# Optimization experiments

Hardware: AMD Instinct MI355X
Metric: run time of the kernel (lower is better)

## Reference

```python
import jax, jax.numpy as jnp
import numpy as np

B, L, DN, DE, DD, H = 2, 512, 512, 128, 128, 8
DK, DEH, DDH = DN // H, DE // H, DD // H
F = 2 * DK + DEH + 2 * DDH  # per-head concat feature size (176)
SLOPE = 0.2


def _kaiming(key, out_f, in_f):
    bound = np.sqrt(6.0 / ((1.0 + SLOPE ** 2) * in_f))
    return jax.random.uniform(key, (out_f, in_f), minval=-bound, maxval=bound, dtype=jnp.float32)


def lin(x, w, b):
    y = jnp.einsum('...i,oi->...o', x, w)
    return y if b is None else y + b


def setup_inputs() -> dict:
    key = jax.random.key(0)
    ks = jax.random.split(key, 16)
    inp = {
        'node_representation': jax.random.normal(ks[0], (B, L, DN), dtype=jnp.float32),
        'edge_representation': jax.random.normal(ks[1], (B, L, L, DE), dtype=jnp.float32),
        'diff_vec': jax.random.normal(ks[2], (B, L, DD), dtype=jnp.float32),
        'Wn_w': _kaiming(ks[3], DN, DN), 'Wn_b': jnp.zeros((DN,), jnp.float32),
        'We_w': _kaiming(ks[4], DE, DE), 'We_b': jnp.zeros((DE,), jnp.float32),
        'Wd_w': _kaiming(ks[5], DD, DD), 'Wd_b': jnp.zeros((DD,), jnp.float32),
        'Wh_w': _kaiming(ks[6], DK, DK), 'Wh_b': jnp.zeros((DK,), jnp.float32),
        'attn_w': _kaiming(ks[7], 1, F),
        'outn_w': _kaiming(ks[8], DN, DN), 'outn_b': jnp.zeros((DN,), jnp.float32),
        'Wn2_w': _kaiming(ks[9], DN, DN), 'Wn2_b': jnp.zeros((DN,), jnp.float32),
        'We2_w': _kaiming(ks[10], DE, DE), 'We2_b': jnp.zeros((DE,), jnp.float32),
        'Wd2_w': _kaiming(ks[11], DD, DD), 'Wd2_b': jnp.zeros((DD,), jnp.float32),
        'edge_w': _kaiming(ks[12], DEH, F), 'edge_b': jnp.zeros((DEH,), jnp.float32),
        'oute_w': _kaiming(ks[13], DE, DE), 'oute_b': jnp.zeros((DE,), jnp.float32),
    }
    return inp


def reference(node_representation, edge_representation, diff_vec,
              Wn_w, Wn_b, We_w, We_b, Wd_w, Wd_b, Wh_w, Wh_b, attn_w,
              outn_w, outn_b, Wn2_w, Wn2_b, We2_w, We2_b, Wd2_w, Wd2_b,
              edge_w, edge_b, oute_w, oute_b):
    lrelu = lambda x: jax.nn.leaky_relu(x, SLOPE)

    # ---- node update (GAT-style with concat score decomposed per term) ----
    npj = lin(node_representation, Wn_w, Wn_b).reshape(B, L, H, DK)
    epj = lin(edge_representation, We_w, We_b).reshape(B, L, L, H, DEH)
    dpj = lin(diff_vec, Wd_w, Wd_b).reshape(B, L, H, DDH)
    a = attn_w[0]  # concat order: [hi, hj, edge, di, dj]
    a_hi, a_hj = a[:DK], a[DK:2 * DK]
    a_e = a[2 * DK:2 * DK + DEH]
    a_di, a_dj = a[2 * DK + DEH:2 * DK + DEH + DDH], a[-DDH:]
    # scores[b,i,j,h]
    s = (jnp.einsum('blhd,d->blh', npj, a_hi)[:, :, None, :]
         + jnp.einsum('blhd,d->blh', npj, a_hj)[:, None, :, :]
         + jnp.einsum('blmhe,e->blmh', epj, a_e)
         + jnp.einsum('blhd,d->blh', dpj, a_di)[:, :, None, :]
         + jnp.einsum('blhd,d->blh', dpj, a_dj)[:, None, :, :])
    diag = jnp.eye(L, dtype=bool)[None, :, :, None]
    s = jnp.where(diag, -jnp.inf, s)
    probs = jax.nn.softmax(lrelu(s), axis=2)  # softmax over j
    node_wh = lin(npj, Wh_w, Wh_b)  # [B,L,H,DK]
    agg = jnp.einsum('blmh,bmhd->blhd', probs, node_wh)
    new_node = (npj + lrelu(agg)).reshape(B, L, DN)
    new_node = lin(new_node, outn_w, outn_b)

    # ---- edge update (concat-linear decomposed into per-term matmuls) ----
    np2 = lin(new_node, Wn2_w, Wn2_b).reshape(B, L, H, DK)
    ep2 = lin(edge_representation, We2_w, We2_b).reshape(B, L, L, H, DEH)
    dp2 = lin(diff_vec, Wd2_w, Wd2_b).reshape(B, L, H, DDH)
    # edge concat order: [edge, hi, hj, di, dj]
    W_e = edge_w[:, :DEH]
    W_hi = edge_w[:, DEH:DEH + DK]
    W_hj = edge_w[:, DEH + DK:DEH + 2 * DK]
    W_di = edge_w[:, DEH + 2 * DK:DEH + 2 * DK + DDH]
    W_dj = edge_w[:, -DDH:]
    e_out = (jnp.einsum('blmhe,fe->blmhf', ep2, W_e)
             + jnp.einsum('blhd,fd->blhf', np2, W_hi)[:, :, None]
             + jnp.einsum('blhd,fd->blhf', np2, W_hj)[:, None]
             + jnp.einsum('blhd,fd->blhf', dp2, W_di)[:, :, None]
             + jnp.einsum('blhd,fd->blhf', dp2, W_dj)[:, None]
             + edge_b)
    new_edge = lin(e_out.reshape(B, L, L, DE), oute_w, oute_b)
    return new_node, new_edge
```

## Files before the change

kernel.cpp:

```cpp
#include <hip/hip_runtime.h>
#include <hip/hip_bf16.h>

typedef unsigned short u16;
typedef unsigned short u16x8 __attribute__((ext_vector_type(8)));
typedef __bf16 bf16x8 __attribute__((ext_vector_type(8)));
typedef float f32x4 __attribute__((ext_vector_type(4)));

#define LRS 0.2f

__device__ __forceinline__ u16 f2b(float f) {
  __hip_bfloat16 h = __float2bfloat16(f);
  return __builtin_bit_cast(u16, h);
}

template<int K, int O, int KSEG>
__device__ __forceinline__ void gemm_rows4(const float* xr, const float* W, const float* bias,
                                           float* yl, float* yg, int ygstride) {
  constexpr int KPT = K / KSEG;
  constexpr int OPP = 256 / KSEG;
  const int t = threadIdx.x;
  const int ks = t % KSEG;
  const int oi = t / KSEG;
#pragma unroll
  for (int pass = 0; pass < O / OPP; ++pass) {
    const int o = pass * OPP + oi;
    float a0 = 0, a1 = 0, a2 = 0, a3 = 0;
    const float* wp = W + (size_t)o * K + ks * KPT;
    const float* xb = xr + ks * KPT;
#pragma unroll 4
    for (int kc = 0; kc < KPT; kc += 4) {
      f32x4 w4 = *(const f32x4*)(wp + kc);
      const float* xp = xb + kc;
#pragma unroll
      for (int j = 0; j < 4; ++j) {
        float w = w4[j];
        a0 += xp[j] * w;
        a1 += xp[K + j] * w;
        a2 += xp[2 * K + j] * w;
        a3 += xp[3 * K + j] * w;
      }
    }
#pragma unroll
    for (int d = 1; d < KSEG; d <<= 1) {
      a0 += __shfl_xor(a0, d, 64);
      a1 += __shfl_xor(a1, d, 64);
      a2 += __shfl_xor(a2, d, 64);
      a3 += __shfl_xor(a3, d, 64);
    }
    if (ks == 0) {
      float bv = bias ? bias[o] : 0.0f;
      float v0 = a0 + bv, v1 = a1 + bv, v2 = a2 + bv, v3 = a3 + bv;
      if (yl) { yl[o] = v0; yl[O + o] = v1; yl[2 * O + o] = v2; yl[3 * O + o] = v3; }
      if (yg) { yg[o] = v0; yg[ygstride + o] = v1; yg[2 * (size_t)ygstride + o] = v2; yg[3 * (size_t)ygstride + o] = v3; }
    }
  }
}

__global__ __launch_bounds__(256) void kW1(const float* We_w, const float* We_b, const float* attn,
                                           const float* We2_w, const float* We2_b,
                                           const float* edge_w, const float* edge_b,
                                           float* Mfull, u16* vb, float* cbe, float* sconst) {
  int gid = blockIdx.x * 256 + threadIdx.x;
  if (gid < 16384) {
    int hf = gid >> 7, c = gid & 127;
    int h = hf >> 4, fo = hf & 15;
    float s = 0;
    for (int e = 0; e < 16; ++e)
      s += edge_w[fo * 176 + e] * We2_w[(h * 16 + e) * 128 + c];
    Mfull[hf * 128 + c] = s;
  } else if (gid < 16384 + 2048) {
    int idx = gid - 16384;
    int c = idx >> 4, hc = idx & 15;
    float s = 0;
    if (hc < 8)
      for (int e = 0; e < 16; ++e)
        s += We_w[(hc * 16 + e) * 128 + c] * attn[128 + e];
    vb[c * 16 + hc] = f2b(s);
  } else if (gid < 18432 + 128) {
    int hf = gid - 18432;
    int h = hf >> 4, fo = hf & 15;
    float s = edge_b[fo];
    for (int e = 0; e < 16; ++e)
      s += We2_b[h * 16 + e] * edge_w[fo * 176 + e];
    cbe[hf] = s;
  } else if (gid < 18560 + 8) {
    int h = gid - 18560;
    float s = 0;
    for (int e = 0; e < 16; ++e)
      s += We_b[h * 16 + e] * attn[128 + e];
    sconst[h] = s;
  }
}

__global__ __launch_bounds__(256) void kW2(const float* oute_w, const float* Mfull, u16* Gb) {
  int gid = blockIdx.x * 256 + threadIdx.x;
  int o = gid >> 7, c = gid & 127;
  float s = 0;
  for (int k = 0; k < 128; ++k)
    s += oute_w[o * 128 + k] * Mfull[k * 128 + c];
  Gb[o * 128 + c] = f2b(s);
}

__global__ __launch_bounds__(256) void kN1(const float* node, const float* diff,
                                           const float* Wn_w, const float* Wn_b,
                                           const float* Wd_w, const float* Wd_b,
                                           const float* Wh_w, const float* Wh_b,
                                           const float* attn, const float* sconst,
                                           float* npj_g, float* nwh_g,
                                           float* srow_g, float* scol_g) {
  __shared__ float nrow[4 * 512], npjl[4 * 512], drow[4 * 128], dpjl[4 * 128];
  const int t = threadIdx.x;
  const int r0 = blockIdx.x * 4;
  *(f32x4*)&nrow[t * 8]     = *(const f32x4*)(node + (size_t)r0 * 512 + t * 8);
  *(f32x4*)&nrow[t * 8 + 4] = *(const f32x4*)(node + (size_t)r0 * 512 + t * 8 + 4);
  if (t < 64) {
    *(f32x4*)&drow[t * 8]     = *(const f32x4*)(diff + (size_t)r0 * 128 + t * 8);
    *(f32x4*)&drow[t * 8 + 4] = *(const f32x4*)(diff + (size_t)r0 * 128 + t * 8 + 4);
  }
  __syncthreads();
  gemm_rows4<512, 512, 4>(nrow, Wn_w, Wn_b, npjl, npj_g + (size_t)r0 * 512, 512);
  gemm_rows4<128, 128, 4>(drow, Wd_w, Wd_b, dpjl, nullptr, 0);
  __syncthreads();
  {
    int d = t & 63, hh = t >> 6;
#pragma unroll
    for (int hi = 0; hi < 2; ++hi) {
      int h = hh + hi * 4;
      float wb = Wh_b[d];
      float acc[4] = {wb, wb, wb, wb};
      for (int k = 0; k < 64; ++k) {
        float w = Wh_w[d * 64 + k];
#pragma unroll
        for (int r = 0; r < 4; ++r) acc[r] += npjl[r * 512 + h * 64 + k] * w;
      }
#pragma unroll
      for (int r = 0; r < 4; ++r) nwh_g[(size_t)(r0 + r) * 512 + h * 64 + d] = acc[r];
    }
  }
  if (t < 32) {
    int r = t >> 3, h = t & 7;
    float shi = 0, shj = 0, sdi = 0, sdj = 0;
    for (int d = 0; d < 64; ++d) {
      float x = npjl[r * 512 + h * 64 + d];
      shi += x * attn[d];
      shj += x * attn[64 + d];
    }
    for (int e = 0; e < 16; ++e) {
      float x = dpjl[r * 128 + h * 16 + e];
      sdi += x * attn[144 + e];
      sdj += x * attn[160 + e];
    }
    srow_g[(r0 + r) * 8 + h] = shi + sdi + sconst[h];
    scol_g[(r0 + r) * 8 + h] = shj + sdj;
  }
}

__global__ __launch_bounds__(256) void kA(const float* edge, const float* npj, const float* nwh,
                                          const float* srow, const float* scol,
                                          const u16* vb, float* nnp) {
  __shared__ float s_arr[512][9];
  __shared__ float red[256];
  __shared__ float mxh[8], inv8[8];
  __shared__ float part[2][512];
  const int bl = blockIdx.x;
  const int b = bl >> 9, l = bl & 511;
  const int t = threadIdx.x;
  const int w = t >> 6, lane = t & 63;
  const int colL = lane & 15, kg = lane >> 4;
  bf16x8 bfr[4];
#pragma unroll
  for (int ks = 0; ks < 4; ++ks) {
    u16x8 u;
#pragma unroll
    for (int j = 0; j < 8; ++j) u[j] = vb[(ks * 32 + kg * 8 + j) * 16 + colL];
    bfr[ks] = __builtin_bit_cast(bf16x8, u);
  }
  float srh = (colL < 8) ? srow[(size_t)bl * 8 + colL] : 0.0f;
  const float* erow = edge + (size_t)bl * 512 * 128;
  for (int fr = 0; fr < 8; ++fr) {
    int m0 = w * 128 + fr * 16;
    f32x4 acc = {0, 0, 0, 0};
#pragma unroll
    for (int ks = 0; ks < 4; ++ks) {
      const float* ep = erow + (size_t)(m0 + colL) * 128 + ks * 32 + kg * 8;
      f32x4 e0 = *(const f32x4*)(ep);
      f32x4 e1 = *(const f32x4*)(ep + 4);
      u16x8 a8;
#pragma unroll
      for (int j = 0; j < 4; ++j) { a8[j] = f2b(e0[j]); a8[4 + j] = f2b(e1[j]); }
      acc = __builtin_amdgcn_mfma_f32_16x16x32_bf16(__builtin_bit_cast(bf16x8, a8), bfr[ks], acc, 0, 0, 0);
    }
    if (colL < 8) {
#pragma unroll
      for (int r = 0; r < 4; ++r) {
        int m = m0 + kg * 4 + r;
        float sv = acc[r] + srh + scol[((size_t)b * 512 + m) * 8 + colL];
        sv = (m == l) ? -__builtin_inff() : (sv >= 0.0f ? sv : LRS * sv);
        s_arr[m][colL] = sv;
      }
    }
  }
  __syncthreads();
  const int h = t & 7, seg = t >> 3;
  float mx = -__builtin_inff();
#pragma unroll 4
  for (int i = 0; i < 16; ++i) mx = fmaxf(mx, s_arr[seg * 16 + i][h]);
  red[t] = mx;
  __syncthreads();
  if (t < 8) {
    float m2 = -__builtin_inff();
    for (int sg = 0; sg < 32; ++sg) m2 = fmaxf(m2, red[sg * 8 + t]);
    mxh[t] = m2;
  }
  __syncthreads();
  float mh = mxh[h];
  float sm = 0;
#pragma unroll 4
  for (int i = 0; i < 16; ++i) {
    int m = seg * 16 + i;
    float p = __expf(s_arr[m][h] - mh);
    s_arr[m][h] = p;
    sm += p;
  }
  red[t] = sm;
  __syncthreads();
  if (t < 8) {
    float s2 = 0;
    for (int sg = 0; sg < 32; ++sg) s2 += red[sg * 8 + t];
    inv8[t] = 1.0f / s2;
  }
  __syncthreads();
  const int half = t >> 7, oq = t & 127;
  const int o4 = oq * 4, hh = oq >> 4;
  f32x4 acc4 = {0, 0, 0, 0};
  const float* nb = nwh + (size_t)b * 512 * 512;
  for (int m = half * 256; m < half * 256 + 256; ++m) {
    float p = s_arr[m][hh];
    f32x4 nv = *(const f32x4*)(nb + (size_t)m * 512 + o4);
    acc4 += p * nv;
  }
  *(f32x4*)&part[half][o4] = acc4;
  __syncthreads();
  if (t < 128) {
    int ob = t * 4, h2 = t >> 4;
    f32x4 s0 = *(f32x4*)&part[0][ob];
    f32x4 s1 = *(f32x4*)&part[1][ob];
    f32x4 np4 = *(const f32x4*)(npj + (size_t)bl * 512 + ob);
    float iv = inv8[h2];
    f32x4 o;
#pragma unroll
    for (int j = 0; j < 4; ++j) {
      float a = (s0[j] + s1[j]) * iv;
      a = a >= 0.0f ? a : LRS * a;
      o[j] = np4[j] + a;
    }
    *(f32x4*)(nnp + (size_t)bl * 512 + ob) = o;
  }
}

__global__ __launch_bounds__(256) void kN2(const float* nnp, const float* outn_w, const float* outn_b,
                                           float* out0) {
  __shared__ float xr[4 * 512];
  const int t = threadIdx.x;
  const int r0 = blockIdx.x * 4;
  *(f32x4*)&xr[t * 4]        = *(const f32x4*)(nnp + (size_t)r0 * 512 + t * 4);
  *(f32x4*)&xr[1024 + t * 4] = *(const f32x4*)(nnp + (size_t)r0 * 512 + 1024 + t * 4);
  __syncthreads();
  gemm_rows4<512, 512, 4>(xr, outn_w, outn_b, nullptr, out0 + (size_t)r0 * 512, 512);
}

__global__ __launch_bounds__(256) void kN3(const float* nn, const float* diff,
                                           const float* Wn2_w, const float* Wn2_b,
                                           const float* Wd2_w, const float* Wd2_b,
                                           const float* edge_w, const float* cbe,
                                           float* Rl_g, float* Rm_g) {
  __shared__ float xr[4 * 512], np2l[4 * 512], dr[4 * 128], dp2l[4 * 128];
  const int t = threadIdx.x;
  const int r0 = blockIdx.x * 4;
  *(f32x4*)&xr[t * 4]        = *(const f32x4*)(nn + (size_t)r0 * 512 + t * 4);
  *(f32x4*)&xr[1024 + t * 4] = *(const f32x4*)(nn + (size_t)r0 * 512 + 1024 + t * 4);
  if (t < 64) {
    *(f32x4*)&dr[t * 8]     = *(const f32x4*)(diff + (size_t)r0 * 128 + t * 8);
    *(f32x4*)&dr[t * 8 + 4] = *(const f32x4*)(diff + (size_t)r0 * 128 + t * 8 + 4);
  }
  __syncthreads();
  gemm_rows4<512, 512, 4>(xr, Wn2_w, Wn2_b, np2l, nullptr, 0);
  gemm_rows4<128, 128, 4>(dr, Wd2_w, Wd2_b, dp2l, nullptr, 0);
  __syncthreads();
  {
    int hf = t & 127, which = t >> 7;
    int h = hf >> 4, fo = hf & 15;
    const float* wh = edge_w + fo * 176 + 16 + which * 64;
    const float* wd = edge_w + fo * 176 + 144 + which * 16;
    float add = which ? 0.0f : cbe[hf];
    float* dst = which ? Rm_g : Rl_g;
#pragma unroll
    for (int r = 0; r < 4; ++r) {
      float a = add;
      for (int d = 0; d < 64; ++d) a += np2l[r * 512 + h * 64 + d] * wh[d];
      for (int e = 0; e < 16; ++e) a += dp2l[r * 128 + h * 16 + e] * wd[e];
      dst[(size_t)(r0 + r) * 128 + hf] = a;
    }
  }
}

__global__ __launch_bounds__(256) void kN4(const float* Rl, const float* Rm,
                                           const float* oute_w, const float* oute_b,
                                           float* Pl, float* Pm) {
  __shared__ float xl[4 * 128], xm[4 * 128];
  const int t = threadIdx.x;
  const int r0 = blockIdx.x * 4;
  if (t < 128) *(f32x4*)&xl[t * 4] = *(const f32x4*)(Rl + (size_t)r0 * 128 + t * 4);
  else { int q = t - 128; *(f32x4*)&xm[q * 4] = *(const f32x4*)(Rm + (size_t)r0 * 128 + q * 4); }
  __syncthreads();
  gemm_rows4<128, 128, 4>(xl, oute_w, oute_b, nullptr, Pl + (size_t)r0 * 128, 128);
  gemm_rows4<128, 128, 4>(xm, oute_w, nullptr, nullptr, Pm + (size_t)r0 * 128, 128);
}

__global__ __launch_bounds__(256) void kE(const float* edge, const u16* Gb,
                                          const float* Pl, const float* Pm, float* oute) {
  __shared__ u16 At[16384];
  __shared__ u16 Gt[16384];
  const int tile = blockIdx.x;
  const int bl = tile >> 2;
  const int b = bl >> 9;
  const int m0 = (tile & 3) * 128;
  const int t = threadIdx.x, lane = t & 63, w = t >> 6;
  const float* Ab = edge + ((size_t)bl * 512 + m0) * 128;
#pragma unroll
  for (int j = 0; j < 8; ++j) {
    int u = j * 256 + t;
    int row = u >> 4, cu = u & 15;
    int su = row * 16 + (cu ^ (row & 7));
    f32x4 e0 = *(const f32x4*)(Ab + (size_t)row * 128 + cu * 8);
    f32x4 e1 = *(const f32x4*)(Ab + (size_t)row * 128 + cu * 8 + 4);
    u16x8 a8;
#pragma unroll
    for (int j2 = 0; j2 < 4; ++j2) { a8[j2] = f2b(e0[j2]); a8[4 + j2] = f2b(e1[j2]); }
    *(u16x8*)(At + su * 8) = a8;
    *(u16x8*)(Gt + su * 8) = *(const u16x8*)(Gb + u * 8);
  }
  __syncthreads();
  const int wr = w >> 1, wc = w & 1;
  const int colL = lane & 15, kg = lane >> 4;
  f32x4 acc[4][4] = {};
#pragma unroll
  for (int ks = 0; ks < 4; ++ks) {
    bf16x8 af[4], bfv[4];
    int cu = ks * 4 + kg;
#pragma unroll
    for (int i = 0; i < 4; ++i) {
      int row = wr * 64 + i * 16 + colL;
      af[i] = *(bf16x8*)(At + (row * 16 + (cu ^ (row & 7))) * 8);
      int orow = wc * 64 + i * 16 + colL;
      bfv[i] = *(bf16x8*)(Gt + (orow * 16 + (cu ^ (orow & 7))) * 8);
    }
#pragma unroll
    for (int i = 0; i < 4; ++i)
#pragma unroll
      for (int n = 0; n < 4; ++n)
        acc[i][n] = __builtin_amdgcn_mfma_f32_16x16x32_bf16(af[i], bfv[n], acc[i][n], 0, 0, 0);
  }
  const float* plp = Pl + (size_t)bl * 128;
  float plv[4];
#pragma unroll
  for (int n = 0; n < 4; ++n) plv[n] = plp[wc * 64 + n * 16 + colL];
  float* ob = oute + ((size_t)bl * 512 + m0) * 128;
#pragma unroll
  for (int i = 0; i < 4; ++i) {
#pragma unroll
    for (int r = 0; r < 4; ++r) {
      int m = wr * 64 + i * 16 + kg * 4 + r;
      const float* pmp = Pm + ((size_t)b * 512 + m0 + m) * 128;
#pragma unroll
      for (int n = 0; n < 4; ++n) {
        int o = wc * 64 + n * 16 + colL;
        ob[(size_t)m * 128 + o] = acc[i][n][r] + plv[n] + pmp[o];
      }
    }
  }
}

extern "C" void kernel_launch(void* const* d_in, const int* in_sizes, int n_in,
                              void* d_out, int out_size, void* d_ws, size_t ws_size,
                              hipStream_t stream) {
  (void)in_sizes; (void)n_in; (void)out_size; (void)ws_size;
  const float* node   = (const float*)d_in[0];
  const float* edge   = (const float*)d_in[1];
  const float* diff   = (const float*)d_in[2];
  const float* Wn_w   = (const float*)d_in[3];
  const float* Wn_b   = (const float*)d_in[4];
  const float* We_w   = (const float*)d_in[5];
  const float* We_b   = (const float*)d_in[6];
  const float* Wd_w   = (const float*)d_in[7];
  const float* Wd_b   = (const float*)d_in[8];
  const float* Wh_w   = (const float*)d_in[9];
  const float* Wh_b   = (const float*)d_in[10];
  const float* attn   = (const float*)d_in[11];
  const float* outn_w = (const float*)d_in[12];
  const float* outn_b = (const float*)d_in[13];
  const float* Wn2_w  = (const float*)d_in[14];
  const float* Wn2_b  = (const float*)d_in[15];
  const float* We2_w  = (const float*)d_in[16];
  const float* We2_b  = (const float*)d_in[17];
  const float* Wd2_w  = (const float*)d_in[18];
  const float* Wd2_b  = (const float*)d_in[19];
  const float* edge_w = (const float*)d_in[20];
  const float* edge_b = (const float*)d_in[21];
  const float* oute_w = (const float*)d_in[22];
  const float* oute_b = (const float*)d_in[23];

  float* out0 = (float*)d_out;
  float* out1 = out0 + 524288;

  float* f = (float*)d_ws;
  size_t off = 0;
  auto alloc = [&](size_t n) { float* p = f + off; off += (n + 7) & ~(size_t)7; return p; };
  float* npj    = alloc(524288);
  float* nwh    = alloc(524288);
  float* srow   = alloc(8192);
  float* scol   = alloc(8192);
  float* sconst = alloc(8);
  float* cbe    = alloc(128);
  float* Mfull  = alloc(16384);
  float* nnp    = alloc(524288);
  float* Rl     = alloc(131072);
  float* Rm     = alloc(131072);
  float* Pl     = alloc(131072);
  float* Pm     = alloc(131072);
  u16* vb = (u16*)(f + off); off += 1024;
  u16* Gb = (u16*)(f + off); off += 8192;

  hipLaunchKernelGGL(kW1, dim3(73), dim3(256), 0, stream,
                     We_w, We_b, attn, We2_w, We2_b, edge_w, edge_b, Mfull, vb, cbe, sconst);
  hipLaunchKernelGGL(kW2, dim3(64), dim3(256), 0, stream, oute_w, Mfull, Gb);
  hipLaunchKernelGGL(kN1, dim3(256), dim3(256), 0, stream,
                     node, diff, Wn_w, Wn_b, Wd_w, Wd_b, Wh_w, Wh_b, attn, sconst,
                     npj, nwh, srow, scol);
  hipLaunchKernelGGL(kA, dim3(1024), dim3(256), 0, stream,
                     edge, npj, nwh, srow, scol, vb, nnp);
  hipLaunchKernelGGL(kN2, dim3(256), dim3(256), 0, stream, nnp, outn_w, outn_b, out0);
  hipLaunchKernelGGL(kN3, dim3(256), dim3(256), 0, stream,
                     out0, diff, Wn2_w, Wn2_b, Wd2_w, Wd2_b, edge_w, cbe, Rl, Rm);
  hipLaunchKernelGGL(kN4, dim3(256), dim3(256), 0, stream, Rl, Rm, oute_w, oute_b, Pl, Pm);
  hipLaunchKernelGGL(kE, dim3(4096), dim3(256), 0, stream, edge, Gb, Pl, Pm, out1);
}
```

Measured before the change: 445.8 us.

## Use fp32 FMA edge scores in kA and double-buffer edge tiles in kE

kA drops the bf16 MFMA edge-score path and computes the per-head edge scores with fp32 FMAs and shuffle reductions, prefetching the next edge row while computing. The leaky-relu and masking step moves into the max pass, and the weighted sum over nodes is split across two accumulators. kE now runs one block per row l, looping over 8 tiles of 64 rows with a double-buffered LDS A-tile and register prefetch, so Gt is loaded once per block instead of four times and loads overlap with MFMA. Risks are lower occupancy and more VALU work in kA, and fewer blocks in kE.

After: 494.0 us. 1.11x slower.

```diff
diff --git a/kernel.cpp b/kernel.cpp
--- a/kernel.cpp
+++ b/kernel.cpp
@@ -59,7 +59,7 @@
 __global__ __launch_bounds__(256) void kW1(const float* We_w, const float* We_b, const float* attn,
                                            const float* We2_w, const float* We2_b,
                                            const float* edge_w, const float* edge_b,
-                                           float* Mfull, u16* vb, float* cbe, float* sconst) {
+                                           float* Mfull, float* vf, float* cbe, float* sconst) {
   int gid = blockIdx.x * 256 + threadIdx.x;
   if (gid < 16384) {
     int hf = gid >> 7, c = gid & 127;
@@ -71,11 +71,12 @@
   } else if (gid < 16384 + 2048) {
     int idx = gid - 16384;
     int c = idx >> 4, hc = idx & 15;
-    float s = 0;
-    if (hc < 8)
+    if (hc < 8) {
+      float s = 0;
       for (int e = 0; e < 16; ++e)
         s += We_w[(hc * 16 + e) * 128 + c] * attn[128 + e];
-    vb[c * 16 + hc] = f2b(s);
+      vf[c * 8 + hc] = s;
+    }
   } else if (gid < 18432 + 128) {
     int hf = gid - 18432;
     int h = hf >> 4, fo = hf & 15;
@@ -157,7 +158,7 @@
 
 __global__ __launch_bounds__(256) void kA(const float* edge, const float* npj, const float* nwh,
                                           const float* srow, const float* scol,
-                                          const u16* vb, float* nnp) {
+                                          const float* vf, float* nnp) {
   __shared__ float s_arr[512][9];
   __shared__ float red[256];
   __shared__ float mxh[8], inv8[8];
@@ -165,46 +166,60 @@
   const int bl = blockIdx.x;
   const int b = bl >> 9, l = bl & 511;
   const int t = threadIdx.x;
-  const int w = t >> 6, lane = t & 63;
-  const int colL = lane & 15, kg = lane >> 4;
-  bf16x8 bfr[4];
-#pragma unroll
-  for (int ks = 0; ks < 4; ++ks) {
-    u16x8 u;
-#pragma unroll
-    for (int j = 0; j < 8; ++j) u[j] = vb[(ks * 32 + kg * 8 + j) * 16 + colL];
-    bfr[ks] = __builtin_bit_cast(bf16x8, u);
-  }
-  float srh = (colL < 8) ? srow[(size_t)bl * 8 + colL] : 0.0f;
-  const float* erow = edge + (size_t)bl * 512 * 128;
-  for (int fr = 0; fr < 8; ++fr) {
-    int m0 = w * 128 + fr * 16;
-    f32x4 acc = {0, 0, 0, 0};
-#pragma unroll
-    for (int ks = 0; ks < 4; ++ks) {
-      const float* ep = erow + (size_t)(m0 + colL) * 128 + ks * 32 + kg * 8;
-      f32x4 e0 = *(const f32x4*)(ep);
-      f32x4 e1 = *(const f32x4*)(ep + 4);
-      u16x8 a8;
-#pragma unroll
-      for (int j = 0; j < 4; ++j) { a8[j] = f2b(e0[j]); a8[4 + j] = f2b(e1[j]); }
-      acc = __builtin_amdgcn_mfma_f32_16x16x32_bf16(__builtin_bit_cast(bf16x8, a8), bfr[ks], acc, 0, 0, 0);
-    }
-    if (colL < 8) {
-#pragma unroll
-      for (int r = 0; r < 4; ++r) {
-        int m = m0 + kg * 4 + r;
-        float sv = acc[r] + srh + scol[((size_t)b * 512 + m) * 8 + colL];
-        sv = (m == l) ? -__builtin_inff() : (sv >= 0.0f ? sv : LRS * sv);
-        s_arr[m][colL] = sv;
-      }
-    }
-  }
-  __syncthreads();
+
+  {
+    const int sub = t & 15, rg = t >> 4;
+    f32x4 vrx[16];
+#pragma unroll
+    for (int q = 0; q < 16; ++q) vrx[q] = *(const f32x4*)(vf + sub * 64 + q * 4);
+    const float* ebase = edge + (size_t)bl * 65536 + (size_t)rg * 128 + sub * 8;
+    f32x4 c0 = *(const f32x4*)ebase;
+    f32x4 c1 = *(const f32x4*)(ebase + 4);
+    for (int it = 0; it < 32; ++it) {
+      f32x4 n0, n1;
+      if (it < 31) {
+        const float* ep = ebase + (size_t)(it + 1) * 2048;
+        n0 = *(const f32x4*)ep;
+        n1 = *(const f32x4*)(ep + 4);
+      }
+      float acc[8];
+#pragma unroll
+      for (int h2 = 0; h2 < 8; ++h2) acc[h2] = 0.0f;
+#pragma unroll
+      for (int j = 0; j < 4; ++j) {
+#pragma unroll
+        for (int h2 = 0; h2 < 8; ++h2) {
+          acc[h2] += c0[j] * vrx[j * 2 + (h2 >> 2)][h2 & 3];
+          acc[h2] += c1[j] * vrx[8 + j * 2 + (h2 >> 2)][h2 & 3];
+        }
+      }
+#pragma unroll
+      for (int d = 1; d < 16; d <<= 1) {
+#pragma unroll
+        for (int h2 = 0; h2 < 8; ++h2) acc[h2] += __shfl_xor(acc[h2], d, 64);
+      }
+      if (sub < 8) {
+        float a = acc[0];
+#pragma unroll
+        for (int h2 = 1; h2 < 8; ++h2) if (sub == h2) a = acc[h2];
+        s_arr[it * 16 + rg][sub] = a;
+      }
+      if (it < 31) { c0 = n0; c1 = n1; }
+    }
+  }
+  __syncthreads();
+
   const int h = t & 7, seg = t >> 3;
+  const float srh2 = srow[(size_t)bl * 8 + h];
   float mx = -__builtin_inff();
 #pragma unroll 4
-  for (int i = 0; i < 16; ++i) mx = fmaxf(mx, s_arr[seg * 16 + i][h]);
+  for (int i = 0; i < 16; ++i) {
+    int m = seg * 16 + i;
+    float sv = s_arr[m][h] + srh2 + scol[((size_t)b * 512 + m) * 8 + h];
+    sv = (m == l) ? -__builtin_inff() : (sv >= 0.0f ? sv : LRS * sv);
+    s_arr[m][h] = sv;
+    mx = fmaxf(mx, sv);
+  }
   red[t] = mx;
   __syncthreads();
   if (t < 8) {
@@ -230,16 +245,16 @@
     inv8[t] = 1.0f / s2;
   }
   __syncthreads();
+
   const int half = t >> 7, oq = t & 127;
   const int o4 = oq * 4, hh = oq >> 4;
-  f32x4 acc4 = {0, 0, 0, 0};
+  f32x4 acc4a = {0, 0, 0, 0}, acc4b = {0, 0, 0, 0};
   const float* nb = nwh + (size_t)b * 512 * 512;
-  for (int m = half * 256; m < half * 256 + 256; ++m) {
-    float p = s_arr[m][hh];
-    f32x4 nv = *(const f32x4*)(nb + (size_t)m * 512 + o4);
-    acc4 += p * nv;
-  }
-  *(f32x4*)&part[half][o4] = acc4;
+  for (int m = half * 256; m < half * 256 + 256; m += 2) {
+    acc4a += s_arr[m][hh]     * *(const f32x4*)(nb + (size_t)m * 512 + o4);
+    acc4b += s_arr[m + 1][hh] * *(const f32x4*)(nb + (size_t)(m + 1) * 512 + o4);
+  }
+  *(f32x4*)&part[half][o4] = acc4a + acc4b;
   __syncthreads();
   if (t < 128) {
     int ob = t * 4, h2 = t >> 4;
@@ -319,65 +334,92 @@
 
 __global__ __launch_bounds__(256) void kE(const float* edge, const u16* Gb,
                                           const float* Pl, const float* Pm, float* oute) {
-  __shared__ u16 At[16384];
   __shared__ u16 Gt[16384];
-  const int tile = blockIdx.x;
-  const int bl = tile >> 2;
+  __shared__ u16 At[2][8192];
+  const int bl = blockIdx.x;
   const int b = bl >> 9;
-  const int m0 = (tile & 3) * 128;
   const int t = threadIdx.x, lane = t & 63, w = t >> 6;
-  const float* Ab = edge + ((size_t)bl * 512 + m0) * 128;
-#pragma unroll
-  for (int j = 0; j < 8; ++j) {
-    int u = j * 256 + t;
+  const float* Ab = edge + (size_t)bl * 65536;
+  const int arow = t >> 2, aseg = t & 3;
+
+  f32x4 pf[8];
+  auto issueA = [&](int tile) {
+    const float* p = Ab + (size_t)(tile * 64 + arow) * 128 + aseg * 32;
+#pragma unroll
+    for (int q = 0; q < 8; ++q) pf[q] = *(const f32x4*)(p + q * 4);
+  };
+  auto writeA = [&](int buf) {
+#pragma unroll
+    for (int jj = 0; jj < 4; ++jj) {
+      u16x8 a8;
+#pragma unroll
+      for (int j2 = 0; j2 < 4; ++j2) {
+        a8[j2]     = f2b(pf[2 * jj][j2]);
+        a8[4 + j2] = f2b(pf[2 * jj + 1][j2]);
+      }
+      int cu = aseg * 4 + jj;
+      *(u16x8*)(At[buf] + (arow * 16 + (cu ^ (arow & 7))) * 8) = a8;
+    }
+  };
+
+  issueA(0);
+#pragma unroll
+  for (int i2 = 0; i2 < 8; ++i2) {
+    int u = i2 * 256 + t;
     int row = u >> 4, cu = u & 15;
-    int su = row * 16 + (cu ^ (row & 7));
-    f32x4 e0 = *(const f32x4*)(Ab + (size_t)row * 128 + cu * 8);
-    f32x4 e1 = *(const f32x4*)(Ab + (size_t)row * 128 + cu * 8 + 4);
-    u16x8 a8;
-#pragma unroll
-    for (int j2 = 0; j2 < 4; ++j2) { a8[j2] = f2b(e0[j2]); a8[4 + j2] = f2b(e1[j2]); }
-    *(u16x8*)(At + su * 8) = a8;
-    *(u16x8*)(Gt + su * 8) = *(const u16x8*)(Gb + u * 8);
-  }
-  __syncthreads();
+    *(u16x8*)(Gt + (row * 16 + (cu ^ (row & 7))) * 8) = *(const u16x8*)(Gb + u * 8);
+  }
+  writeA(0);
+  __syncthreads();
+
   const int wr = w >> 1, wc = w & 1;
   const int colL = lane & 15, kg = lane >> 4;
-  f32x4 acc[4][4] = {};
-#pragma unroll
-  for (int ks = 0; ks < 4; ++ks) {
-    bf16x8 af[4], bfv[4];
-    int cu = ks * 4 + kg;
-#pragma unroll
-    for (int i = 0; i < 4; ++i) {
-      int row = wr * 64 + i * 16 + colL;
-      af[i] = *(bf16x8*)(At + (row * 16 + (cu ^ (row & 7))) * 8);
-      int orow = wc * 64 + i * 16 + colL;
-      bfv[i] = *(bf16x8*)(Gt + (orow * 16 + (cu ^ (orow & 7))) * 8);
-    }
-#pragma unroll
-    for (int i = 0; i < 4; ++i)
-#pragma unroll
-      for (int n = 0; n < 4; ++n)
-        acc[i][n] = __builtin_amdgcn_mfma_f32_16x16x32_bf16(af[i], bfv[n], acc[i][n], 0, 0, 0);
-  }
   const float* plp = Pl + (size_t)bl * 128;
   float plv[4];
 #pragma unroll
   for (int n = 0; n < 4; ++n) plv[n] = plp[wc * 64 + n * 16 + colL];
-  float* ob = oute + ((size_t)bl * 512 + m0) * 128;
-#pragma unroll
-  for (int i = 0; i < 4; ++i) {
-#pragma unroll
-    for (int r = 0; r < 4; ++r) {
-      int m = wr * 64 + i * 16 + kg * 4 + r;
-      const float* pmp = Pm + ((size_t)b * 512 + m0 + m) * 128;
+
+  for (int tile = 0; tile < 8; ++tile) {
+    if (tile < 7) issueA(tile + 1);
+    const int buf = tile & 1;
+    f32x4 acc[2][4] = {};
+#pragma unroll
+    for (int ks = 0; ks < 4; ++ks) {
+      int cu = ks * 4 + kg;
+      bf16x8 af[2], bfv[4];
+#pragma unroll
+      for (int i = 0; i < 2; ++i) {
+        int row = wr * 32 + i * 16 + colL;
+        af[i] = *(bf16x8*)(At[buf] + (row * 16 + (cu ^ (row & 7))) * 8);
+      }
 #pragma unroll
       for (int n = 0; n < 4; ++n) {
-        int o = wc * 64 + n * 16 + colL;
-        ob[(size_t)m * 128 + o] = acc[i][n][r] + plv[n] + pmp[o];
-      }
-    }
+        int orow = wc * 64 + n * 16 + colL;
+        bfv[n] = *(bf16x8*)(Gt + (orow * 16 + (cu ^ (orow & 7))) * 8);
+      }
+#pragma unroll
+      for (int i = 0; i < 2; ++i)
+#pragma unroll
+        for (int n = 0; n < 4; ++n)
+          acc[i][n] = __builtin_amdgcn_mfma_f32_16x16x32_bf16(af[i], bfv[n], acc[i][n], 0, 0, 0);
+    }
+    if (tile < 7) writeA(buf ^ 1);
+    const int m0 = tile * 64;
+    float* ob = oute + ((size_t)bl * 512 + m0) * 128;
+#pragma unroll
+    for (int i = 0; i < 2; ++i) {
+#pragma unroll
+      for (int r = 0; r < 4; ++r) {
+        int m = wr * 32 + i * 16 + kg * 4 + r;
+        const float* pmp = Pm + ((size_t)b * 512 + m0 + m) * 128;
+#pragma unroll
+        for (int n = 0; n < 4; ++n) {
+          int o = wc * 64 + n * 16 + colL;
+          ob[(size_t)m * 128 + o] = acc[i][n][r] + plv[n] + pmp[o];
+        }
+      }
+    }
+    __syncthreads();
   }
 }
 
@@ -428,20 +470,20 @@
   float* Rm     = alloc(131072);
   float* Pl     = alloc(131072);
   float* Pm     = alloc(131072);
-  u16* vb = (u16*)(f + off); off += 1024;
+  float* vf     = alloc(1024);
   u16* Gb = (u16*)(f + off); off += 8192;
 
   hipLaunchKernelGGL(kW1, dim3(73), dim3(256), 0, stream,
-                     We_w, We_b, attn, We2_w, We2_b, edge_w, edge_b, Mfull, vb, cbe, sconst);
+                     We_w, We_b, attn, We2_w, We2_b, edge_w, edge_b, Mfull, vf, cbe, sconst);
   hipLaunchKernelGGL(kW2, dim3(64), dim3(256), 0, stream, oute_w, Mfull, Gb);
   hipLaunchKernelGGL(kN1, dim3(256), dim3(256), 0, stream,
                      node, diff, Wn_w, Wn_b, Wd_w, Wd_b, Wh_w, Wh_b, attn, sconst,
                      npj, nwh, srow, scol);
   hipLaunchKernelGGL(kA, dim3(1024), dim3(256), 0, stream,
-                     edge, npj, nwh, srow, scol, vb, nnp);
+                     edge, npj, nwh, srow, scol, vf, nnp);
   hipLaunchKernelGGL(kN2, dim3(256), dim3(256), 0, stream, nnp, outn_w, outn_b, out0);
   hipLaunchKernelGGL(kN3, dim3(256), dim3(256), 0, stream,
                      out0, diff, Wn2_w, Wn2_b, Wd2_w, Wd2_b, edge_w, cbe, Rl, Rm);
   hipLaunchKernelGGL(kN4, dim3(256), dim3(256), 0, stream, Rl, Rm, oute_w, oute_b, Pl, Pm);
-  hipLaunchKernelGGL(kE, dim3(4096), dim3(256), 0, stream, edge, Gb, Pl, Pm, out1);
-}
+  hipLaunchKernelGGL(kE, dim3(1024), dim3(256), 0, stream, edge, Gb, Pl, Pm, out1);
+}
```
